# Optimization experiments

Hardware: AMD Instinct MI355X
Metric: run time of the kernel (lower is better)

Reference implementation:

```python
import jax, jax.numpy as jnp
import numpy as np

EPSILON = 1e-8
B, T, H = 4, 4096, 2048          # batch, seq, hidden_dim
D, NH, K = 256, 4, 32            # belief_dim, num_heads, top_k
NB, NG = 65536, 16               # n_beliefs, n_goals
NEG_INF = -1e30


def setup_inputs() -> dict:
    key = jax.random.key(0)
    ks = jax.random.split(key, 8)
    hidden = jax.random.normal(ks[0], (B, T, H), dtype=jnp.float32)
    beliefs = jax.random.normal(ks[1], (NB, D), dtype=jnp.float32)
    active_mask = jax.random.bernoulli(ks[2], 0.5, (NB,))
    goal_embeddings = jax.random.normal(ks[3], (NG, D), dtype=jnp.float32)
    goal_priorities = jax.random.uniform(ks[4], (NG,), dtype=jnp.float32)
    # torch nn.Linear weights are [out_features, in_features]
    Wq = jax.random.normal(ks[5], (NH * D, H), dtype=jnp.float32) / np.float32(np.sqrt(H))
    Wo = jax.random.normal(ks[6], (H, NH * D), dtype=jnp.float32) / np.float32(np.sqrt(NH * D))
    log_temperature = jax.random.normal(ks[7], (NH,), dtype=jnp.float32) * 0.1
    return {"hidden": hidden, "beliefs": beliefs, "active_mask": active_mask,
            "goal_embeddings": goal_embeddings, "goal_priorities": goal_priorities,
            "Wq": Wq, "Wo": Wo, "log_temperature": log_temperature}


def reference(hidden, beliefs, active_mask, goal_embeddings, goal_priorities, Wq, Wo, log_temperature):
    # --- rough-score top-k pre-filter over active beliefs (N_active > top_k path) ---
    mean_query = hidden.mean(axis=(0, 1))                      # [H]
    rough_query = (Wq @ mean_query).reshape(NH, D).mean(axis=0)  # [D]
    radii = jnp.maximum(jnp.linalg.norm(beliefs, axis=-1), EPSILON)  # [NB]
    angles = beliefs / radii[:, None]                          # [NB, D]
    rough_scores = angles @ rough_query                        # [NB]
    # mask-gather: inactive beliefs get -inf so topk selects only active ones
    rough_scores = jnp.where(active_mask, rough_scores, NEG_INF)
    _, topk_idx = jax.lax.top_k(rough_scores, K)               # [K]
    active_beliefs = beliefs[topk_idx]                         # [K, D]

    # --- angle-normalized keys, raw values ---
    a_radii = jnp.maximum(jnp.linalg.norm(active_beliefs, axis=-1), EPSILON)
    keys = active_beliefs / a_radii[:, None]                   # [K, D]
    values = active_beliefs                                    # [K, D]

    # --- per-head queries and temperature ---
    queries = (hidden @ Wq.T).reshape(B, T, NH, D)             # [B,T,h,D]
    temperature = jnp.maximum(jnp.exp(log_temperature), 0.1)   # [h]
    scores = jnp.einsum('bthd,nd->bthn', queries, keys) / np.float32(np.sqrt(D))
    scores = scores * temperature[None, None, :, None]         # [B,T,h,K]

    # --- goal-similarity bias ---
    g_radii = jnp.maximum(jnp.linalg.norm(goal_embeddings, axis=-1), EPSILON)
    goal_angles = goal_embeddings / g_radii[:, None]           # [NG, D]
    sim = (keys @ goal_angles.T) * goal_priorities[None, :]    # [K, NG]
    goal_bias = sim.max(axis=-1)                               # [K], same for all heads
    scores = scores + goal_bias[None, None, None, :]

    attn = jax.nn.softmax(scores, axis=-1)                     # [B,T,h,K]
    retrieved = jnp.einsum('bthn,nd->bthd', attn, values).reshape(B, T, NH * D)
    return retrieved @ Wo.T                                    # [B,T,H]
```

## Files before the change

### kernel.cpp

```cpp
#include <hip/hip_runtime.h>

typedef unsigned int u32;
typedef unsigned short u16;
typedef unsigned long long u64;

typedef __bf16 bf16x8 __attribute__((ext_vector_type(8)));
typedef float f32x4 __attribute__((ext_vector_type(4)));

#define DEV __device__ __forceinline__

DEV u16 f2bf(float f) {
  u32 u = __float_as_uint(f);
  u += 0x7fffu + ((u >> 16) & 1u);
  return (u16)(u >> 16);
}
DEV float bf2f(u16 u) { return __uint_as_float((u32)u << 16); }

DEV void gld_lds16(const void* g, void* l) {
  __builtin_amdgcn_global_load_lds((const __attribute__((address_space(1))) u32*)g,
                                   (__attribute__((address_space(3))) u32*)l, 16, 0, 0);
}

DEV u64 packkey(float f, u32 idx) {
  u32 u = __float_as_uint(f);
  u = (u & 0x80000000u) ? ~u : (u | 0x80000000u);
  return ((u64)u << 32) | (u32)(~idx);
}

__global__ __launch_bounds__(256) void k_conv_mean(const float4* __restrict__ hidden4,
                                                   ushort4* __restrict__ hb4,
                                                   float4* __restrict__ partial4) {
  const int c4 = blockIdx.x * 256 + threadIdx.x;
  const int r0 = blockIdx.y * 64;
  float4 s = {0.f, 0.f, 0.f, 0.f};
  for (int r = 0; r < 64; r++) {
    float4 v = hidden4[(size_t)(r0 + r) * 512 + c4];
    ushort4 o; o.x = f2bf(v.x); o.y = f2bf(v.y); o.z = f2bf(v.z); o.w = f2bf(v.w);
    hb4[(size_t)(r0 + r) * 512 + c4] = o;
    s.x += v.x; s.y += v.y; s.z += v.z; s.w += v.w;
  }
  partial4[blockIdx.y * 512 + c4] = s;
}

__global__ __launch_bounds__(256) void k_mean(const float* __restrict__ partial,
                                              float* __restrict__ mean) {
  __shared__ float red[256];
  const int t = threadIdx.x;
  const int c = t & 15, s = t >> 4;
  const int col = blockIdx.x * 16 + c;
  float acc = 0.f;
  for (int ch = s; ch < 256; ch += 16) acc += partial[ch * 2048 + col];
  red[t] = acc;
  __syncthreads();
  for (int st = 8; st > 0; st >>= 1) {
    if (s < st) red[t] += red[t + st * 16];
    __syncthreads();
  }
  if (s == 0) mean[col] = red[c] * (1.0f / 16384.0f);
}

__global__ __launch_bounds__(256) void k_rq(const float* __restrict__ Wq,
                                            const float* __restrict__ mean,
                                            float* __restrict__ rq) {
  const int w = threadIdx.x >> 6, l = threadIdx.x & 63;
  const int row = blockIdx.x * 4 + w;
  float s = 0.f;
#pragma unroll
  for (int j = 0; j < 32; j++)
    s = fmaf(Wq[(size_t)row * 2048 + j * 64 + l], mean[j * 64 + l], s);
  for (int mk = 1; mk < 64; mk <<= 1) s += __shfl_xor(s, mk);
  if (l == 0) atomicAdd(&rq[row & 255], 0.25f * s);
}

__global__ __launch_bounds__(256) void k_rough(const float* __restrict__ beliefs,
                                               const void* __restrict__ amask,
                                               const float* __restrict__ rq,
                                               u64* __restrict__ keys) {
  const int t = threadIdx.x, w = t >> 6, l = t & 63;
  const int n = blockIdx.x * 4 + w;
  u32 mv = ((const u32*)amask)[l];
  bool isInt = (__ballot(mv > 1u) == 0ull);
  float4 b = *(const float4*)(beliefs + (size_t)n * 256 + l * 4);
  float4 qv = *(const float4*)(rq + l * 4);
  float dot = b.x * qv.x + b.y * qv.y + b.z * qv.z + b.w * qv.w;
  float ss = b.x * b.x + b.y * b.y + b.z * b.z + b.w * b.w;
  for (int mk = 1; mk < 64; mk <<= 1) { dot += __shfl_xor(dot, mk); ss += __shfl_xor(ss, mk); }
  if (l == 0) {
    bool act = isInt ? (((const int*)amask)[n] != 0)
                     : (((const unsigned char*)amask)[n] != 0);
    float score = act ? dot / fmaxf(sqrtf(ss), 1e-8f) : -1e30f;
    keys[n] = packkey(score, (u32)n);
  }
}

__global__ __launch_bounds__(256) void k_top1(const u64* __restrict__ keys,
                                              u64* __restrict__ cands) {
  __shared__ u64 ws[128];
  const int t = threadIdx.x, w = t >> 6, l = t & 63;
  const u64* src = keys + (size_t)blockIdx.x * 1024;
  u64 v0 = src[t], v1 = src[t + 256], v2 = src[t + 512], v3 = src[t + 768];
  for (int r = 0; r < 32; r++) {
    u64 a = v0 > v1 ? v0 : v1;
    u64 b = v2 > v3 ? v2 : v3;
    u64 m = a > b ? a : b;
#pragma unroll
    for (int mk = 1; mk < 64; mk <<= 1) { u64 o = __shfl_xor(m, mk); m = o > m ? o : m; }
    if (l == 0) ws[w * 32 + r] = m;
    v0 = (v0 == m) ? 0ull : v0;
    v1 = (v1 == m) ? 0ull : v1;
    v2 = (v2 == m) ? 0ull : v2;
    v3 = (v3 == m) ? 0ull : v3;
  }
  __syncthreads();
  if (w == 0) {
    u64 u0 = ws[l], u1 = ws[64 + l];
    for (int r = 0; r < 32; r++) {
      u64 m = u0 > u1 ? u0 : u1;
#pragma unroll
      for (int mk = 1; mk < 64; mk <<= 1) { u64 o = __shfl_xor(m, mk); m = o > m ? o : m; }
      if (l == 0) cands[blockIdx.x * 32 + r] = m;
      u0 = (u0 == m) ? 0ull : u0;
      u1 = (u1 == m) ? 0ull : u1;
    }
  }
}

__global__ __launch_bounds__(256) void k_top2_prep(const u64* __restrict__ cands,
                                                   const float* __restrict__ beliefs,
                                                   const float* __restrict__ goals,
                                                   const float* __restrict__ prio,
                                                   const float* __restrict__ logt,
                                                   float* __restrict__ keysf_g,
                                                   float* __restrict__ valsf_g,
                                                   float* __restrict__ biasO,
                                                   float* __restrict__ tempO) {
  __shared__ u64 ws[128];
  __shared__ int idxS[32];
  __shared__ float keysf[32 * 256];
  __shared__ float gradS[16];
  const int t = threadIdx.x, w = t >> 6, l = t & 63;
  u64 v[8];
#pragma unroll
  for (int i = 0; i < 8; i++) v[i] = cands[t + i * 256];
  for (int r = 0; r < 32; r++) {
    u64 m = v[0];
#pragma unroll
    for (int i = 1; i < 8; i++) m = v[i] > m ? v[i] : m;
#pragma unroll
    for (int mk = 1; mk < 64; mk <<= 1) { u64 o = __shfl_xor(m, mk); m = o > m ? o : m; }
    if (l == 0) ws[w * 32 + r] = m;
#pragma unroll
    for (int i = 0; i < 8; i++) v[i] = (v[i] == m) ? 0ull : v[i];
  }
  __syncthreads();
  if (w == 0) {
    u64 u0 = ws[l], u1 = ws[64 + l];
    for (int r = 0; r < 32; r++) {
      u64 m = u0 > u1 ? u0 : u1;
#pragma unroll
      for (int mk = 1; mk < 64; mk <<= 1) { u64 o = __shfl_xor(m, mk); m = o > m ? o : m; }
      if (l == 0) idxS[r] = (int)(~(u32)(m & 0xffffffffull));
      u0 = (u0 == m) ? 0ull : u0;
      u1 = (u1 == m) ? 0ull : u1;
    }
  }
  __syncthreads();
  for (int g = w * 4; g < w * 4 + 4; g++) {
    float4 gv = *(const float4*)(goals + g * 256 + l * 4);
    float ss = gv.x * gv.x + gv.y * gv.y + gv.z * gv.z + gv.w * gv.w;
    for (int mk = 1; mk < 64; mk <<= 1) ss += __shfl_xor(ss, mk);
    if (l == 0) gradS[g] = fmaxf(sqrtf(ss), 1e-8f);
  }
  for (int kk = w * 8; kk < w * 8 + 8; kk++) {
    int idx = idxS[kk];
    float4 bv = *(const float4*)(beliefs + (size_t)idx * 256 + l * 4);
    float ss = bv.x * bv.x + bv.y * bv.y + bv.z * bv.z + bv.w * bv.w;
    for (int mk = 1; mk < 64; mk <<= 1) ss += __shfl_xor(ss, mk);
    float rr = 1.0f / fmaxf(sqrtf(ss), 1e-8f);
    float4 kv; kv.x = bv.x * rr; kv.y = bv.y * rr; kv.z = bv.z * rr; kv.w = bv.w * rr;
    *(float4*)&keysf[kk * 256 + l * 4] = kv;
    *(float4*)&keysf_g[kk * 256 + l * 4] = kv;
    *(float4*)&valsf_g[kk * 256 + l * 4] = bv;
  }
  __syncthreads();
  for (int kk = w * 8; kk < w * 8 + 8; kk++) {
    float4 kv = *(const float4*)&keysf[kk * 256 + l * 4];
    float best = -1e30f;
    for (int g = 0; g < 16; g++) {
      float4 gv = *(const float4*)(goals + g * 256 + l * 4);
      float d = kv.x * gv.x + kv.y * gv.y + kv.z * gv.z + kv.w * gv.w;
      for (int mk = 1; mk < 64; mk <<= 1) d += __shfl_xor(d, mk);
      float sim = d / gradS[g] * prio[g];
      best = fmaxf(best, sim);
    }
    if (l == 0) biasO[kk] = best;
  }
  if (t < 4) tempO[t] = fmaxf(__expf(logt[t]), 0.1f);
}

__global__ __launch_bounds__(256) void k_build(const float* __restrict__ Wq,
                                               const float* __restrict__ Wo,
                                               const float* __restrict__ keysf_g,
                                               const float* __restrict__ valsf_g,
                                               u16* __restrict__ Kp,
                                               u16* __restrict__ VWoT) {
  __shared__ __align__(16) float sbuf[16384];
  const int t = threadIdx.x;
  if (blockIdx.x < 128) {
    float* keysS = sbuf;
    float* WqS = sbuf + 8192;
    const int h = blockIdx.x >> 5;
    const int c0 = (blockIdx.x & 31) * 64;
#pragma unroll
    for (int it = 0; it < 32; it++) keysS[t + it * 256] = keysf_g[t + it * 256];
    const int n0 = (t >> 5) * 4;
    const int c2 = (t & 31) * 2;
    float acc[4][2] = {};
    for (int dc = 0; dc < 4; dc++) {
      __syncthreads();
#pragma unroll
      for (int it = 0; it < 16; it++) {
        int i = t + it * 256;
        int r = i >> 6, c = i & 63;
        WqS[i] = Wq[(size_t)(h * 256 + dc * 64 + r) * 2048 + c0 + c];
      }
      __syncthreads();
      for (int d4 = 0; d4 < 16; d4++) {
        float4 kv[4];
#pragma unroll
        for (int i = 0; i < 4; i++)
          kv[i] = *(const float4*)&keysS[(n0 + i) * 256 + dc * 64 + d4 * 4];
#pragma unroll
        for (int dd = 0; dd < 4; dd++) {
          float2 w2 = *(const float2*)&WqS[(d4 * 4 + dd) * 64 + c2];
          float kvd[4] = {kv[0][dd], kv[1][dd], kv[2][dd], kv[3][dd]};
#pragma unroll
          for (int i = 0; i < 4; i++) {
            acc[i][0] = fmaf(kvd[i], w2.x, acc[i][0]);
            acc[i][1] = fmaf(kvd[i], w2.y, acc[i][1]);
          }
        }
      }
    }
#pragma unroll
    for (int i = 0; i < 4; i++) {
      u32 pk = (u32)f2bf(acc[i][0]) | ((u32)f2bf(acc[i][1]) << 16);
      *(u32*)&Kp[(size_t)(h * 32 + n0 + i) * 2048 + c0 + c2] = pk;
    }
  } else {
    float* valsS = sbuf;
    float* WoS = sbuf + 8192;
    const int c0 = (blockIdx.x - 128) * 32;
#pragma unroll
    for (int it = 0; it < 32; it++) valsS[t + it * 256] = valsf_g[t + it * 256];
    const int c = t >> 3;
    const int n0 = (t & 7) * 4;
    for (int h = 0; h < 4; h++) {
      __syncthreads();
#pragma unroll
      for (int it = 0; it < 32; it++) {
        int i = t + it * 256;
        int r = i >> 8, d = i & 255;
        WoS[i] = Wo[(size_t)(c0 + r) * 1024 + h * 256 + d];
      }
      __syncthreads();
      float acc[4] = {};
      for (int d4 = 0; d4 < 64; d4++) {
        float4 w4 = *(const float4*)&WoS[c * 256 + d4 * 4];
#pragma unroll
        for (int i = 0; i < 4; i++) {
          float4 kv = *(const float4*)&valsS[(n0 + i) * 256 + d4 * 4];
          acc[i] = fmaf(w4.x, kv.x, acc[i]);
          acc[i] = fmaf(w4.y, kv.y, acc[i]);
          acc[i] = fmaf(w4.z, kv.z, acc[i]);
          acc[i] = fmaf(w4.w, kv.w, acc[i]);
        }
      }
      ushort4 o; o.x = f2bf(acc[0]); o.y = f2bf(acc[1]); o.z = f2bf(acc[2]); o.w = f2bf(acc[3]);
      *(ushort4*)&VWoT[(size_t)(c0 + c) * 128 + h * 32 + n0] = o;
    }
  }
}

__global__ __launch_bounds__(512) void k_attn(const u16* __restrict__ hb,
                                              const u16* __restrict__ kp,
                                              const u16* __restrict__ vwot,
                                              const float* __restrict__ bias,
                                              const float* __restrict__ temp,
                                              float* __restrict__ out) {
  __shared__ __align__(16) u16 smem[32768];
  u16* Plds = smem + 24576;
  const int t = threadIdx.x;
  const int w = t >> 6, l = t & 63;
  const int q = l >> 4, c = l & 15;
  const int m0 = blockIdx.x * 64;
  const int rh = w >> 2, hd = w & 3;

  const int rowA = t >> 3;
  const int cbA = (t & 7) ^ (rowA & 7);
  const u16* srcA = hb + (size_t)(m0 + rowA) * 2048 + cbA * 8;
  const int rowB1 = 64 + rowA;
  const int cbB0 = (t & 7) ^ (rowA & 7);
  const int cbB1 = (t & 7) ^ (rowB1 & 7);
  const u16* srcB0 = kp + (size_t)rowA * 2048 + cbB0 * 8;
  const u16* srcB1 = kp + (size_t)rowB1 * 2048 + cbB1 * 8;
  u16* dstA = smem + w * 512;
  u16* dstB0 = smem + 8192 + w * 512;
  u16* dstB1 = smem + 8192 + 4096 + w * 512;

  f32x4 acc[2][2] = {};
  gld_lds16(srcA, dstA);
  gld_lds16(srcB0, dstB0);
  gld_lds16(srcB1, dstB1);
  __syncthreads();
  int buf = 0;
  for (int s = 0; s < 32; s++) {
    if (s < 31) {
      const int kt = (s + 1) * 64;
      const int bo = buf ^ 1;
      gld_lds16(srcA + kt, dstA + bo * 4096);
      gld_lds16(srcB0 + kt, dstB0 + bo * 8192);
      gld_lds16(srcB1 + kt, dstB1 + bo * 8192);
    }
    const u16* Ab = smem + buf * 4096;
    const u16* Bb = smem + 8192 + buf * 8192;
    bf16x8 af[2][2], bfr[2][2];
#pragma unroll
    for (int mi = 0; mi < 2; mi++) {
      const int ra = rh * 32 + mi * 16 + c;
#pragma unroll
      for (int ks = 0; ks < 2; ks++)
        af[mi][ks] = __builtin_bit_cast(bf16x8,
            *(const uint4*)&Ab[ra * 64 + (((ks * 4 + q) ^ (ra & 7)) * 8)]);
    }
#pragma unroll
    for (int ni = 0; ni < 2; ni++) {
      const int rb = hd * 32 + ni * 16 + c;
#pragma unroll
      for (int ks = 0; ks < 2; ks++)
        bfr[ni][ks] = __builtin_bit_cast(bf16x8,
            *(const uint4*)&Bb[rb * 64 + (((ks * 4 + q) ^ (rb & 7)) * 8)]);
    }
#pragma unroll
    for (int ks = 0; ks < 2; ks++)
#pragma unroll
      for (int mi = 0; mi < 2; mi++)
#pragma unroll
        for (int ni = 0; ni < 2; ni++)
          acc[mi][ni] = __builtin_amdgcn_mfma_f32_16x16x32_bf16(af[mi][ks], bfr[ni][ks],
                                                                acc[mi][ni], 0, 0, 0);
    __syncthreads();
    buf ^= 1;
  }

  const int rowV = t >> 4;
  const int sltV = t & 15;
  const int rowV1 = 32 + rowV;
  const u16* srcV0 = vwot + (size_t)rowV * 128 + ((sltV ^ (rowV & 7)) * 8);
  const u16* srcV1 = vwot + (size_t)rowV1 * 128 + ((sltV ^ (rowV1 & 7)) * 8);
  u16* dstV0 = smem + w * 512;
  u16* dstV1 = smem + 4096 + w * 512;
  gld_lds16(srcV0, dstV0);
  gld_lds16(srcV1, dstV1);

  const float ts = temp[hd] * 0.0625f;
  const float b0 = bias[c], b1 = bias[16 + c];
#pragma unroll
  for (int mi = 0; mi < 2; mi++) {
#pragma unroll
    for (int r = 0; r < 4; r++) {
      float v0 = fmaf(acc[mi][0][r], ts, b0);
      float v1 = fmaf(acc[mi][1][r], ts, b1);
      float m = fmaxf(v0, v1);
#pragma unroll
      for (int mk = 1; mk <= 8; mk <<= 1) m = fmaxf(m, __shfl_xor(m, mk));
      float e0 = __expf(v0 - m), e1 = __expf(v1 - m);
      float sum = e0 + e1;
#pragma unroll
      for (int mk = 1; mk <= 8; mk <<= 1) sum += __shfl_xor(sum, mk);
      float inv = 1.0f / sum;
      const int rp = rh * 32 + mi * 16 + q * 4 + r;
      const int k0 = hd * 32 + c, k1 = k0 + 16;
      Plds[rp * 128 + (((k0 >> 3) ^ (rp & 7)) * 8) + (k0 & 7)] = f2bf(e0 * inv);
      Plds[rp * 128 + (((k1 >> 3) ^ (rp & 7)) * 8) + (k1 & 7)] = f2bf(e1 * inv);
    }
  }
  __syncthreads();

  const int rw = w & 3, chh = w >> 2;
  int vbuf = 0;
  for (int cb = 0; cb < 32; cb++) {
    if (cb < 31) {
      const size_t so = (size_t)(cb + 1) * 8192;
      const int bo = vbuf ^ 1;
      gld_lds16(srcV0 + so, dstV0 + bo * 8192);
      gld_lds16(srcV1 + so, dstV1 + bo * 8192);
    }
    const u16* Vb = smem + vbuf * 8192;
    f32x4 oacc[2] = {};
    const int rp = rw * 16 + c;
#pragma unroll
    for (int ks = 0; ks < 4; ks++) {
      bf16x8 pa = __builtin_bit_cast(bf16x8,
          *(const uint4*)&Plds[rp * 128 + (((ks * 4 + q) ^ (rp & 7)) * 8)]);
#pragma unroll
      for (int ni = 0; ni < 2; ni++) {
        const int rv = chh * 32 + ni * 16 + c;
        bf16x8 vb = __builtin_bit_cast(bf16x8,
            *(const uint4*)&Vb[rv * 128 + (((ks * 4 + q) ^ (rv & 7)) * 8)]);
        oacc[ni] = __builtin_amdgcn_mfma_f32_16x16x32_bf16(pa, vb, oacc[ni], 0, 0, 0);
      }
    }
#pragma unroll
    for (int ni = 0; ni < 2; ni++) {
      const int col = cb * 64 + chh * 32 + ni * 16 + c;
#pragma unroll
      for (int r = 0; r < 4; r++)
        out[(size_t)(m0 + rw * 16 + q * 4 + r) * 2048 + col] = oacc[ni][r];
    }
    __syncthreads();
    vbuf ^= 1;
  }
}

extern "C" void kernel_launch(void* const* d_in, const int* in_sizes, int n_in,
                              void* d_out, int out_size, void* d_ws, size_t ws_size,
                              hipStream_t stream) {
  const float* hidden = (const float*)d_in[0];
  const float* beliefs = (const float*)d_in[1];
  const void* amask = d_in[2];
  const float* goals = (const float*)d_in[3];
  const float* prio = (const float*)d_in[4];
  const float* Wq = (const float*)d_in[5];
  const float* Wo = (const float*)d_in[6];
  const float* logt = (const float*)d_in[7];
  float* out = (float*)d_out;

  char* ws = (char*)d_ws;
  size_t off = 0;
  auto alloc = [&](size_t bytes) { char* p = ws + off; off = (off + bytes + 255) & ~(size_t)255; return p; };
  u16* hb      = (u16*)alloc(67108864);
  u16* kp      = (u16*)alloc(524288);
  u16* vwot    = (u16*)alloc(524288);
  float* partial = (float*)alloc(2097152);
  float* meanq = (float*)alloc(8192);
  float* rq    = (float*)alloc(1024);
  u64* keys    = (u64*)alloc(524288);
  u64* cands   = (u64*)alloc(16384);
  float* keysf = (float*)alloc(32768);
  float* valsf = (float*)alloc(32768);
  float* biasv = (float*)alloc(128);
  float* tempv = (float*)alloc(16);

  hipMemsetAsync(rq, 0, 1024, stream);
  k_conv_mean<<<dim3(2, 256), 256, 0, stream>>>((const float4*)hidden, (ushort4*)hb, (float4*)partial);
  k_mean<<<128, 256, 0, stream>>>(partial, meanq);
  k_rq<<<256, 256, 0, stream>>>(Wq, meanq, rq);
  k_rough<<<16384, 256, 0, stream>>>(beliefs, amask, rq, keys);
  k_top1<<<64, 256, 0, stream>>>(keys, cands);
  k_top2_prep<<<1, 256, 0, stream>>>(cands, beliefs, goals, prio, logt, keysf, valsf, biasv, tempv);
  k_build<<<192, 256, 0, stream>>>(Wq, Wo, keysf, valsf, kp, vwot);
  k_attn<<<256, 512, 0, stream>>>(hb, kp, vwot, biasv, tempv, out);
}
```

Measured before the change: 513.3 us.

## Deepen attention GEMM pipeline to four LDS stages and stream V directly

The first GEMM loop in k_attn moves from a double-buffered LDS pipeline with two syncthreads per step to a four-stage ring. It prefetches three tiles ahead, uses explicit vmcnt waits and a single barrier per iteration, and raises LDS usage to about 112KB. The second phase keeps P fragments in registers and reads VWoT directly from global memory (likely L2-resident) instead of staging it through LDS, which removes the per-chunk barriers. The trade-offs are higher LDS use, which lowers occupancy, and uncoalesced or unstaged global reads of V.

```diff
diff --git a/kernel.cpp b/kernel.cpp
--- a/kernel.cpp
+++ b/kernel.cpp
@@ -288,13 +288,17 @@
                                               const float* __restrict__ bias,
                                               const float* __restrict__ temp,
                                               float* __restrict__ out) {
-  __shared__ __align__(16) u16 smem[32768];
-  u16* Plds = smem + 24576;
+  __shared__ __align__(16) u16 smem[57344];
+  u16* Plds = smem + 49152;
   const int t = threadIdx.x;
   const int w = t >> 6, l = t & 63;
   const int q = l >> 4, c = l & 15;
   const int m0 = blockIdx.x * 64;
   const int rh = w >> 2, hd = w & 3;
+
+  const float ts = temp[hd] * 0.0625f;
+  const float b0 = bias[c], b1 = bias[16 + c];
+  asm volatile("s_waitcnt vmcnt(0) lgkmcnt(0)" ::: "memory");
 
   const int rowA = t >> 3;
   const int cbA = (t & 7) ^ (rowA & 7);
@@ -305,25 +309,29 @@
   const u16* srcB0 = kp + (size_t)rowA * 2048 + cbB0 * 8;
   const u16* srcB1 = kp + (size_t)rowB1 * 2048 + cbB1 * 8;
   u16* dstA = smem + w * 512;
-  u16* dstB0 = smem + 8192 + w * 512;
-  u16* dstB1 = smem + 8192 + 4096 + w * 512;
+  u16* dstB0 = smem + 16384 + w * 512;
+  u16* dstB1 = smem + 16384 + 4096 + w * 512;
+
+  auto issue3 = [&](int j) {
+    const int bo = j & 3;
+    gld_lds16(srcA + j * 64, dstA + bo * 4096);
+    gld_lds16(srcB0 + j * 64, dstB0 + bo * 8192);
+    gld_lds16(srcB1 + j * 64, dstB1 + bo * 8192);
+  };
 
   f32x4 acc[2][2] = {};
-  gld_lds16(srcA, dstA);
-  gld_lds16(srcB0, dstB0);
-  gld_lds16(srcB1, dstB1);
-  __syncthreads();
-  int buf = 0;
+  issue3(0); issue3(1); issue3(2);
+
   for (int s = 0; s < 32; s++) {
-    if (s < 31) {
-      const int kt = (s + 1) * 64;
-      const int bo = buf ^ 1;
-      gld_lds16(srcA + kt, dstA + bo * 4096);
-      gld_lds16(srcB0 + kt, dstB0 + bo * 8192);
-      gld_lds16(srcB1 + kt, dstB1 + bo * 8192);
-    }
-    const u16* Ab = smem + buf * 4096;
-    const u16* Bb = smem + 8192 + buf * 8192;
+    if (s <= 29)      asm volatile("s_waitcnt vmcnt(6)" ::: "memory");
+    else if (s == 30) asm volatile("s_waitcnt vmcnt(3)" ::: "memory");
+    else              asm volatile("s_waitcnt vmcnt(0)" ::: "memory");
+    __builtin_amdgcn_s_barrier();
+    __builtin_amdgcn_sched_barrier(0);
+    if (s < 29) issue3(s + 3);
+
+    const u16* Ab = smem + (s & 3) * 4096;
+    const u16* Bb = smem + 16384 + (s & 3) * 8192;
     bf16x8 af[2][2], bfr[2][2];
 #pragma unroll
     for (int mi = 0; mi < 2; mi++) {
@@ -341,6 +349,8 @@
         bfr[ni][ks] = __builtin_bit_cast(bf16x8,
             *(const uint4*)&Bb[rb * 64 + (((ks * 4 + q) ^ (rb & 7)) * 8)]);
     }
+    asm volatile("s_waitcnt lgkmcnt(0)" ::: "memory");
+    __builtin_amdgcn_sched_barrier(0);
 #pragma unroll
     for (int ks = 0; ks < 2; ks++)
 #pragma unroll
@@ -349,22 +359,8 @@
         for (int ni = 0; ni < 2; ni++)
           acc[mi][ni] = __builtin_amdgcn_mfma_f32_16x16x32_bf16(af[mi][ks], bfr[ni][ks],
                                                                 acc[mi][ni], 0, 0, 0);
-    __syncthreads();
-    buf ^= 1;
-  }
-
-  const int rowV = t >> 4;
-  const int sltV = t & 15;
-  const int rowV1 = 32 + rowV;
-  const u16* srcV0 = vwot + (size_t)rowV * 128 + ((sltV ^ (rowV & 7)) * 8);
-  const u16* srcV1 = vwot + (size_t)rowV1 * 128 + ((sltV ^ (rowV1 & 7)) * 8);
-  u16* dstV0 = smem + w * 512;
-  u16* dstV1 = smem + 4096 + w * 512;
-  gld_lds16(srcV0, dstV0);
-  gld_lds16(srcV1, dstV1);
-
-  const float ts = temp[hd] * 0.0625f;
-  const float b0 = bias[c], b1 = bias[16 + c];
+  }
+
 #pragma unroll
   for (int mi = 0; mi < 2; mi++) {
 #pragma unroll
@@ -388,27 +384,23 @@
   __syncthreads();
 
   const int rw = w & 3, chh = w >> 2;
-  int vbuf = 0;
+  const int rp = rw * 16 + c;
+  bf16x8 pa[4];
+#pragma unroll
+  for (int ks = 0; ks < 4; ks++)
+    pa[ks] = __builtin_bit_cast(bf16x8,
+        *(const uint4*)&Plds[rp * 128 + (((ks * 4 + q) ^ (rp & 7)) * 8)]);
+
   for (int cb = 0; cb < 32; cb++) {
-    if (cb < 31) {
-      const size_t so = (size_t)(cb + 1) * 8192;
-      const int bo = vbuf ^ 1;
-      gld_lds16(srcV0 + so, dstV0 + bo * 8192);
-      gld_lds16(srcV1 + so, dstV1 + bo * 8192);
-    }
-    const u16* Vb = smem + vbuf * 8192;
     f32x4 oacc[2] = {};
-    const int rp = rw * 16 + c;
-#pragma unroll
-    for (int ks = 0; ks < 4; ks++) {
-      bf16x8 pa = __builtin_bit_cast(bf16x8,
-          *(const uint4*)&Plds[rp * 128 + (((ks * 4 + q) ^ (rp & 7)) * 8)]);
-#pragma unroll
-      for (int ni = 0; ni < 2; ni++) {
-        const int rv = chh * 32 + ni * 16 + c;
-        bf16x8 vb = __builtin_bit_cast(bf16x8,
-            *(const uint4*)&Vb[rv * 128 + (((ks * 4 + q) ^ (rv & 7)) * 8)]);
-        oacc[ni] = __builtin_amdgcn_mfma_f32_16x16x32_bf16(pa, vb, oacc[ni], 0, 0, 0);
+#pragma unroll
+    for (int ni = 0; ni < 2; ni++) {
+      const int rv = cb * 64 + chh * 32 + ni * 16 + c;
+      const u16* vr = vwot + (size_t)rv * 128 + q * 8;
+#pragma unroll
+      for (int ks = 0; ks < 4; ks++) {
+        bf16x8 vb = __builtin_bit_cast(bf16x8, *(const uint4*)(vr + ks * 32));
+        oacc[ni] = __builtin_amdgcn_mfma_f32_16x16x32_bf16(pa[ks], vb, oacc[ni], 0, 0, 0);
       }
     }
 #pragma unroll
@@ -418,8 +410,6 @@
       for (int r = 0; r < 4; r++)
         out[(size_t)(m0 + rw * 16 + q * 4 + r) * 2048 + col] = oacc[ni][r];
     }
-    __syncthreads();
-    vbuf ^= 1;
   }
 }
 
```

New measurement: 527.8 us. 2.8% more time.
